# Kernel tuning notes

Measured on AMD Instinct MI355X. Metric: run time of the kernel, lower is better.

Reference implementation:

```python
import jax, jax.numpy as jnp
import numpy as np

EPS = 1e-5


def _layernorm(x, w, b):
    mu = jnp.mean(x, axis=-1, keepdims=True)
    var = jnp.var(x, axis=-1, keepdims=True)
    return (x - mu) * jax.lax.rsqrt(var + EPS) * w + b


def setup_inputs() -> dict:
    key = jax.random.key(0)
    ks = jax.random.split(key, 3)
    h, dff = 1024, 4096
    x = jax.random.normal(ks[0], (4, 2048, h), dtype=jnp.float32)
    w1 = jax.random.normal(ks[1], (h, dff), dtype=jnp.float32) * (1.0 / np.sqrt(h))
    w2 = jax.random.normal(ks[2], (dff, h), dtype=jnp.float32) * (1.0 / np.sqrt(dff))
    return {
        "x": x,
        "ln1_w": jnp.ones((h,), jnp.float32),
        "ln1_b": jnp.zeros((h,), jnp.float32),
        "ln2_w": jnp.ones((h,), jnp.float32),
        "ln2_b": jnp.zeros((h,), jnp.float32),
        "w1": w1,
        "b1": jnp.zeros((dff,), jnp.float32),
        "w2": w2,
        "b2": jnp.zeros((h,), jnp.float32),
    }


def reference(x, ln1_w, ln1_b, ln2_w, ln2_b, w1, b1, w2, b2):
    # double 1D FFT: over hidden (dim=-1) then sequence (dim=-2), keep real part
    fourier_x = jnp.fft.fft(jnp.fft.fft(x, axis=-1), axis=-2).real
    x = x + fourier_x
    x = _layernorm(x, ln1_w, ln1_b)
    # FFN: Linear -> exact GELU -> Linear (dropout is identity in eval)
    h = jax.nn.gelu(jnp.einsum("bsd,df->bsf", x, w1) + b1, approximate=False)
    x = x + jnp.einsum("bsf,fd->bsd", h, w2) + b2
    return _layernorm(x, ln2_w, ln2_b)
```

## Files before the change

kernel.cpp:

```cpp
#include <hip/hip_runtime.h>
#include <hip/hip_bf16.h>
#include <math.h>

typedef __bf16 bf16_t;
typedef __bf16 bf16x8 __attribute__((ext_vector_type(8)));
typedef __bf16 bf16x4 __attribute__((ext_vector_type(4)));
typedef float  f32x4  __attribute__((ext_vector_type(4)));

#define NROWS 8192
#define HD    1024
#define DFF   4096
#define HKEEP 513

typedef __attribute__((address_space(1))) const void* gas_cptr;
typedef __attribute__((address_space(3))) void* las_ptr;

__device__ __forceinline__ void gload_lds16(const void* g, void* l) {
  __builtin_amdgcn_global_load_lds((gas_cptr)g, (las_ptr)l, 16, 0, 0);
}

template <int N> __device__ __forceinline__ void vmw() {
  if      constexpr (N==4)  asm volatile("s_waitcnt vmcnt(4)"  ::: "memory");
  else if constexpr (N==6)  asm volatile("s_waitcnt vmcnt(6)"  ::: "memory");
}

__global__ __launch_bounds__(256) void transpose_to_bf16(
    const float* __restrict__ in, bf16_t* __restrict__ out, int R, int C)
{
  __shared__ float tile[32][33];
  const int bx = blockIdx.x, by = blockIdx.y;
  const int tx = threadIdx.x, ty = threadIdx.y;
  #pragma unroll
  for (int i = ty; i < 32; i += 8)
    tile[i][tx] = in[(size_t)(by*32 + i)*C + bx*32 + tx];
  __syncthreads();
  #pragma unroll
  for (int i = ty; i < 32; i += 8)
    out[(size_t)(bx*32 + i)*R + by*32 + tx] = (bf16_t)tile[tx][i];
}

#define RPB 16
#define LDW 1036
__global__ __launch_bounds__(512) void fft_h_t(
    const float* __restrict__ x, float* __restrict__ reT, float* __restrict__ imT)
{
  __shared__ float sre[8*LDW], sim[8*LDW], twc[512], tws[512];
  const int t = threadIdx.x;
  const int row0 = blockIdx.x * RPB;
  {
    float sv, cv; sincosf(-6.28318530717958647692f * (float)t * (1.0f/1024.0f), &sv, &cv);
    twc[t] = cv; tws[t] = sv;
  }
  #pragma unroll
  for (int q = 0; q < 4; ++q) {
    const int i = t + 512*q;
    const int pr = i >> 8;
    const int c4 = i & 255;
    float4 vr = *(const float4*)(x + (size_t)(row0 + 2*pr    )*HD + c4*4);
    float4 vi = *(const float4*)(x + (size_t)(row0 + 2*pr + 1)*HD + c4*4);
    *(float4*)&sre[pr*LDW + c4*4] = vr;
    *(float4*)&sim[pr*LDW + c4*4] = vi;
  }
  __syncthreads();
  const int b0i = __brev((unsigned)t) >> 22;
  const int b1i = __brev((unsigned)(t + 512)) >> 22;
  float rv[32];
  #pragma unroll
  for (int q = 0; q < 8; ++q) {
    rv[4*q]   = sre[q*LDW + b0i];
    rv[4*q+1] = sre[q*LDW + b1i];
    rv[4*q+2] = sim[q*LDW + b0i];
    rv[4*q+3] = sim[q*LDW + b1i];
  }
  __syncthreads();
  #pragma unroll
  for (int q = 0; q < 8; ++q) {
    sre[q*LDW + t]       = rv[4*q];
    sre[q*LDW + t + 512] = rv[4*q+1];
    sim[q*LDW + t]       = rv[4*q+2];
    sim[q*LDW + t + 512] = rv[4*q+3];
  }
  __syncthreads();
  for (int s = 0; s < 10; ++s) {
    const int half = 1 << s;
    const int j    = t & (half - 1);
    const int ib   = ((t >> s) << (s + 1)) | j;
    const int ti2  = j << (9 - s);
    const float wc = twc[ti2], ws = tws[ti2];
    #pragma unroll
    for (int q = 0; q < 8; ++q) {
      float* pr = &sre[q*LDW]; float* pi = &sim[q*LDW];
      const float r1 = pr[ib],      i1v = pi[ib];
      const float r2 = pr[ib+half], i2v = pi[ib+half];
      const float tr = r2*wc - i2v*ws;
      const float ti = r2*ws + i2v*wc;
      pr[ib]      = r1 + tr; pi[ib]      = i1v + ti;
      pr[ib+half] = r1 - tr; pi[ib+half] = i1v - ti;
    }
    __syncthreads();
  }
  const int tx = t & 15, th = t >> 4;
  const int q  = tx >> 1, par = tx & 1;
  #pragma unroll
  for (int hh = 0; hh < 17; ++hh) {
    const int h = hh*32 + th;
    if (h < HKEEP) {
      const int mh = (1024 - h) & 1023;
      const float zr = sre[q*LDW + h],  zi = sim[q*LDW + h];
      const float mr = sre[q*LDW + mh], mi = sim[q*LDW + mh];
      float orr, oii;
      if (par == 0) { orr = 0.5f*(zr + mr); oii = 0.5f*(zi - mi); }
      else          { orr = 0.5f*(zi + mi); oii = 0.5f*(mr - zr); }
      reT[(size_t)h*NROWS + row0 + tx] = orr;
      imT[(size_t)h*NROWS + row0 + tx] = oii;
    }
  }
}

__global__ __launch_bounds__(256) void fft_s_col(
    const float* __restrict__ reT, const float* __restrict__ imT,
    float* __restrict__ fT)
{
  __shared__ float sre[2048], sim[2048], twc[1024], tws[1024];
  const int t = threadIdx.x;
  const int h = blockIdx.x;
  const int batch = blockIdx.y;
  const size_t base = (size_t)h * NROWS + batch * 2048;
  for (int k = t; k < 1024; k += 256) {
    float sv, cv; sincosf(-6.28318530717958647692f * (float)k * (1.0f/2048.0f), &sv, &cv);
    twc[k] = cv; tws[k] = sv;
  }
  #pragma unroll
  for (int q = 0; q < 8; ++q) {
    const int i = t + 256*q;
    const int src = __brev((unsigned)i) >> 21;
    sre[i] = reT[base + src];
    sim[i] = imT[base + src];
  }
  __syncthreads();
  for (int s = 0; s < 11; ++s) {
    const int half = 1 << s;
    #pragma unroll
    for (int q = 0; q < 4; ++q) {
      const int b  = t + 256*q;
      const int j  = b & (half - 1);
      const int ib = ((b >> s) << (s + 1)) | j;
      const int ti2 = j << (10 - s);
      const float wc = twc[ti2], ws = tws[ti2];
      const float r1 = sre[ib],       i1v = sim[ib];
      const float r2 = sre[ib+half],  i2v = sim[ib+half];
      const float tr = r2*wc - i2v*ws;
      const float ti = r2*ws + i2v*wc;
      sre[ib]      = r1 + tr; sim[ib]      = i1v + ti;
      sre[ib+half] = r1 - tr; sim[ib+half] = i1v - ti;
    }
    __syncthreads();
  }
  #pragma unroll
  for (int q = 0; q < 8; ++q) {
    const int i = t + 256*q;
    fT[base + i] = sre[i];
  }
}

__global__ __launch_bounds__(256) void umadd_kernel(
    const float* __restrict__ fT, const float* __restrict__ x,
    float* __restrict__ y)
{
  __shared__ float tile[32][33];
  const int h0 = blockIdx.x * 32;
  const int b0 = blockIdx.y * 32;
  const int tx = threadIdx.x, ty = threadIdx.y;
  const int batch = b0 >> 11;
  const int s0    = b0 & 2047;
  #pragma unroll
  for (int i = ty; i < 32; i += 8) {
    const int h = h0 + i;
    float v;
    if (h <= 512) {
      v = fT[(size_t)h * NROWS + b0 + tx];
    } else {
      const int sp = (2048 - (s0 + tx)) & 2047;
      v = fT[(size_t)(1024 - h) * NROWS + (batch << 11) + sp];
    }
    tile[i][tx] = v;
  }
  __syncthreads();
  #pragma unroll
  for (int i = ty; i < 32; i += 8) {
    const size_t gi = (size_t)(b0+i)*HD + h0+tx;
    y[gi] = x[gi] + tile[tx][i];
  }
}

__global__ __launch_bounds__(256) void layernorm_f2b(
    const float* __restrict__ in, const float* __restrict__ gw,
    const float* __restrict__ gb, bf16_t* __restrict__ ob)
{
  __shared__ float red[8];
  const size_t row = blockIdx.x;
  const int t = threadIdx.x;
  const float* xr = in + row * HD;
  float4 v = *(const float4*)(xr + t*4);
  float s = v.x + v.y + v.z + v.w;
  #pragma unroll
  for (int o = 32; o > 0; o >>= 1) s += __shfl_xor(s, o);
  if ((t & 63) == 0) red[t >> 6] = s;
  __syncthreads();
  const float mu = (red[0]+red[1]+red[2]+red[3]) * (1.0f/1024.0f);
  const float dx = v.x-mu, dy = v.y-mu, dz = v.z-mu, dw = v.w-mu;
  float sq = dx*dx + dy*dy + dz*dz + dw*dw;
  #pragma unroll
  for (int o = 32; o > 0; o >>= 1) sq += __shfl_xor(sq, o);
  if ((t & 63) == 0) red[4 + (t >> 6)] = sq;
  __syncthreads();
  const float var  = (red[4]+red[5]+red[6]+red[7]) * (1.0f/1024.0f);
  const float rstd = rsqrtf(var + 1e-5f);
  const float4 wv = *(const float4*)(gw + t*4);
  const float4 bv = *(const float4*)(gb + t*4);
  bf16x4 o;
  o[0] = (bf16_t)(dx*rstd*wv.x + bv.x);
  o[1] = (bf16_t)(dy*rstd*wv.y + bv.y);
  o[2] = (bf16_t)(dz*rstd*wv.z + bv.z);
  o[3] = (bf16_t)(dw*rstd*wv.w + bv.w);
  *(bf16x4*)(ob + row*HD + t*4) = o;
}

__global__ __launch_bounds__(256) void layernorm_b2f(
    const bf16_t* __restrict__ in, const float* __restrict__ gw,
    const float* __restrict__ gb, float* __restrict__ of)
{
  __shared__ float red[8];
  const size_t row = blockIdx.x;
  const int t = threadIdx.x;
  bf16x4 v4 = *(const bf16x4*)(in + row*HD + t*4);
  const float vx = (float)v4[0], vy = (float)v4[1], vz = (float)v4[2], vw = (float)v4[3];
  float s = vx + vy + vz + vw;
  #pragma unroll
  for (int o = 32; o > 0; o >>= 1) s += __shfl_xor(s, o);
  if ((t & 63) == 0) red[t >> 6] = s;
  __syncthreads();
  const float mu = (red[0]+red[1]+red[2]+red[3]) * (1.0f/1024.0f);
  const float dx = vx-mu, dy = vy-mu, dz = vz-mu, dw = vw-mu;
  float sq = dx*dx + dy*dy + dz*dz + dw*dw;
  #pragma unroll
  for (int o = 32; o > 0; o >>= 1) sq += __shfl_xor(sq, o);
  if ((t & 63) == 0) red[4 + (t >> 6)] = sq;
  __syncthreads();
  const float var  = (red[4]+red[5]+red[6]+red[7]) * (1.0f/1024.0f);
  const float rstd = rsqrtf(var + 1e-5f);
  const float4 wv = *(const float4*)(gw + t*4);
  const float4 bv = *(const float4*)(gb + t*4);
  float4 o;
  o.x = dx*rstd*wv.x + bv.x;
  o.y = dy*rstd*wv.y + bv.y;
  o.z = dz*rstd*wv.z + bv.z;
  o.w = dw*rstd*wv.w + bv.w;
  *(float4*)(of + row*HD + t*4) = o;
}

__device__ __forceinline__ float gelu_fast(float v) {
  const float u  = 0.7978845608028654f * v * (1.0f + 0.044715f * v * v);
  const float e  = exp2f(-2.8853900817779268f * u);
  return v / (1.0f + e);
}

template <int NQ, bool GELU_OUT>
__global__ __launch_bounds__(512, 2) void gemm8r(
    const bf16_t* __restrict__ A,
    const bf16_t* __restrict__ Bt,
    const float*  __restrict__ bias,
    const bf16_t* __restrict__ resid,
    bf16_t* __restrict__ outB,
    int M, int N, int K, int gx)
{
  __shared__ bf16_t As[2][2][128*64];
  __shared__ bf16_t Bs[2][2][NQ*64*64];

  const int tid  = threadIdx.x;
  const int wave = tid >> 6, lane = tid & 63;
  const int wr = wave >> 2, wc = wave & 3;
  const int lr = lane & 15, lkg = lane >> 4;

  const int nwg = gridDim.x;
  const int sid = (blockIdx.x & 7) * (nwg >> 3) + (blockIdx.x >> 3);
  const int bx = sid % gx, by = sid / gx;
  const int brow = by * 256, bcol = bx * (NQ*128);

  const int rl = lane >> 3;
  const int sg = (lane & 7) ^ rl;

  auto stageA = [&](int b, int mh, int tt) {
    #pragma unroll
    for (int l = 0; l < 2; ++l) {
      const int row = brow + l*128 + mh*64 + wave*8 + rl;
      gload_lds16(A + (size_t)row * K + tt*64 + sg*8,
                  &As[b][mh][(l*64 + wave*8)*64]);
    }
  };
  auto stageB = [&](int b, int nh, int tt) {
    #pragma unroll
    for (int l = 0; l < NQ; ++l) {
      const int rho = l*64 + wave*8 + rl;
      const int wcs = rho / (NQ*16), r = rho % (NQ*16);
      const int row = bcol + wcs*(NQ*32) + nh*(NQ*16) + r;
      gload_lds16(Bt + (size_t)row * K + tt*64 + sg*8,
                  &Bs[b][nh][(l*64 + wave*8)*64]);
    }
  };

  f32x4 acc[8][2*NQ] = {};
  bf16x8 af[4][2];
  bf16x8 bq[2][NQ][2];

  const int NT = K >> 6;
  const int NI = NT >> 1;
  constexpr int WT = (NQ==2) ? 6 : 4;

  #define PHASE(BUF, MH, NH, DOA, DOB, STG, DOW) do { \
    if constexpr (DOA) { \
      _Pragma("unroll") for (int m = 0; m < 4; ++m) { \
      _Pragma("unroll") for (int ks = 0; ks < 2; ++ks) \
        af[m][ks] = *(const bf16x8*)&As[BUF][MH][(wr*64 + m*16 + lr)*64 + (((lkg + ks*4) ^ (lr & 7)) << 3)]; } \
    } \
    if constexpr (DOB) { \
      _Pragma("unroll") for (int n = 0; n < NQ; ++n) { \
      _Pragma("unroll") for (int ks = 0; ks < 2; ++ks) \
        bq[NH][n][ks] = *(const bf16x8*)&Bs[BUF][NH][(wc*(NQ*16) + n*16 + lr)*64 + (((lkg + ks*4) ^ (lr & 7)) << 3)]; } \
    } \
    STG; \
    __builtin_amdgcn_s_barrier(); \
    asm volatile("s_waitcnt lgkmcnt(0)" ::: "memory"); \
    __builtin_amdgcn_sched_barrier(0); \
    __builtin_amdgcn_s_setprio(1); \
    _Pragma("unroll") for (int m = 0; m < 4; ++m) { \
    _Pragma("unroll") for (int n = 0; n < NQ; ++n) { \
    _Pragma("unroll") for (int ks = 0; ks < 2; ++ks) \
      acc[(MH)*4+m][(NH)*NQ+n] = __builtin_amdgcn_mfma_f32_16x16x32_bf16(bq[NH][n][ks], af[m][ks], acc[(MH)*4+m][(NH)*NQ+n], 0, 0, 0); } } \
    __builtin_amdgcn_s_setprio(0); \
    if constexpr (DOW) vmw<WT>(); \
    __builtin_amdgcn_s_barrier(); \
  } while (0)

  stageB(0,0,0); stageA(0,0,0); stageB(0,1,0); stageA(0,1,0);
  stageB(1,0,1); stageA(1,0,1); stageB(1,1,1);
  vmw<WT>();
  __builtin_amdgcn_s_barrier();

  for (int j = 0; j < NI; ++j) {
    const int c1 = 2*j + 1;
    const int n2 = (2*j + 2 < NT) ? 2*j + 2 : NT - 1;
    const int n3 = (2*j + 3 < NT) ? 2*j + 3 : NT - 1;
    PHASE(0, 0, 0, 1, 1, stageA(1,1,c1), false);
    PHASE(0, 0, 1, 0, 1, stageB(0,0,n2), false);
    PHASE(0, 1, 1, 1, 0, stageA(0,0,n2), false);
    PHASE(0, 1, 0, 0, 0, stageB(0,1,n2), true);
    PHASE(1, 0, 0, 1, 1, stageA(0,1,n2), false);
    PHASE(1, 0, 1, 0, 1, stageB(1,0,n3), false);
    PHASE(1, 1, 1, 1, 0, stageA(1,0,n3), false);
    PHASE(1, 1, 0, 0, 0, stageB(1,1,n3), true);
  }
  #undef PHASE

  #pragma unroll
  for (int im = 0; im < 8; ++im) {
    const int row = brow + wr*128 + (im >> 2)*64 + (im & 3)*16 + lr;
    #pragma unroll
    for (int in = 0; in < 2*NQ; ++in) {
      const int col = bcol + wc*(NQ*32) + (in/NQ)*(NQ*16) + (in%NQ)*16 + lkg*4;
      const float4 bv4 = *(const float4*)(bias + col);
      float v0 = acc[im][in][0] + bv4.x;
      float v1 = acc[im][in][1] + bv4.y;
      float v2 = acc[im][in][2] + bv4.z;
      float v3 = acc[im][in][3] + bv4.w;
      bf16x4 o;
      if constexpr (GELU_OUT) {
        o[0] = (bf16_t)gelu_fast(v0); o[1] = (bf16_t)gelu_fast(v1);
        o[2] = (bf16_t)gelu_fast(v2); o[3] = (bf16_t)gelu_fast(v3);
      } else {
        bf16x4 rr = *(const bf16x4*)(resid + (size_t)row * N + col);
        o[0] = (bf16_t)(v0 + (float)rr[0]); o[1] = (bf16_t)(v1 + (float)rr[1]);
        o[2] = (bf16_t)(v2 + (float)rr[2]); o[3] = (bf16_t)(v3 + (float)rr[3]);
      }
      *(bf16x4*)(outB + (size_t)row * N + col) = o;
    }
  }
}

extern "C" void kernel_launch(void* const* d_in, const int* in_sizes, int n_in,
                              void* d_out, int out_size, void* d_ws, size_t ws_size,
                              hipStream_t stream) {
  const float* x    = (const float*)d_in[0];
  const float* ln1w = (const float*)d_in[1];
  const float* ln1b = (const float*)d_in[2];
  const float* ln2w = (const float*)d_in[3];
  const float* ln2b = (const float*)d_in[4];
  const float* w1   = (const float*)d_in[5];
  const float* b1   = (const float*)d_in[6];
  const float* w2   = (const float*)d_in[7];
  const float* b2   = (const float*)d_in[8];
  float* out = (float*)d_out;

  char* ws = (char*)d_ws;
  bf16_t* w1b = (bf16_t*)(ws);
  bf16_t* w2b = (bf16_t*)(ws + (8u   << 20));
  float*  reT = (float*) (ws + (16u  << 20));
  float*  imT = (float*) (ws + (33u  << 20));
  float*  fT  = (float*) (ws + (50u  << 20));
  float*  y   = (float*) (ws + (67u  << 20));
  bf16_t* xn  = (bf16_t*)(ws + (99u  << 20));
  bf16_t* hg  = (bf16_t*)(ws + (16u  << 20));
  bf16_t* z   = (bf16_t*)(ws + (80u  << 20));

  transpose_to_bf16<<<dim3(DFF/32, HD/32), dim3(32, 8), 0, stream>>>(w1, w1b, HD, DFF);
  transpose_to_bf16<<<dim3(HD/32, DFF/32), dim3(32, 8), 0, stream>>>(w2, w2b, DFF, HD);

  fft_h_t<<<NROWS/RPB, 512, 0, stream>>>(x, reT, imT);

  fft_s_col<<<dim3(513, 4), 256, 0, stream>>>(reT, imT, fT);

  umadd_kernel<<<dim3(HD/32, NROWS/32), dim3(32, 8), 0, stream>>>(fT, x, y);

  layernorm_f2b<<<NROWS, 256, 0, stream>>>(y, ln1w, ln1b, xn);

  gemm8r<2, true><<<(NROWS/256)*(DFF/256), 512, 0, stream>>>(
      xn, w1b, b1, nullptr, hg, NROWS, DFF, HD, DFF/256);
  gemm8r<1, false><<<(NROWS/256)*(HD/128), 512, 0, stream>>>(
      hg, w2b, b2, xn, z, NROWS, HD, DFF, HD/128);

  layernorm_b2f<<<NROWS, 256, 0, stream>>>(z, ln2w, ln2b, out);
}
```

Measured before the change: 286.9 us.

## Fuse FFT unmirror-add with LayerNorm1 and store FFT output in bf16

After: 276.8 us. -3.5%, faster.

```diff
diff --git a/kernel.cpp b/kernel.cpp
--- a/kernel.cpp
+++ b/kernel.cpp
@@ -119,7 +119,7 @@
 
 __global__ __launch_bounds__(256) void fft_s_col(
     const float* __restrict__ reT, const float* __restrict__ imT,
-    float* __restrict__ fT)
+    bf16_t* __restrict__ fTb)
 {
   __shared__ float sre[2048], sim[2048], twc[1024], tws[1024];
   const int t = threadIdx.x;
@@ -159,71 +159,72 @@
   #pragma unroll
   for (int q = 0; q < 8; ++q) {
     const int i = t + 256*q;
-    fT[base + i] = sre[i];
-  }
-}
-
-__global__ __launch_bounds__(256) void umadd_kernel(
-    const float* __restrict__ fT, const float* __restrict__ x,
-    float* __restrict__ y)
-{
-  __shared__ float tile[32][33];
-  const int h0 = blockIdx.x * 32;
-  const int b0 = blockIdx.y * 32;
-  const int tx = threadIdx.x, ty = threadIdx.y;
-  const int batch = b0 >> 11;
-  const int s0    = b0 & 2047;
-  #pragma unroll
-  for (int i = ty; i < 32; i += 8) {
-    const int h = h0 + i;
+    fTb[base + i] = (bf16_t)sre[i];
+  }
+}
+
+#define FLD 1028
+__global__ __launch_bounds__(256) void fuse_umadd_ln1(
+    const bf16_t* __restrict__ fTb, const float* __restrict__ x,
+    const float* __restrict__ gw, const float* __restrict__ gb,
+    bf16_t* __restrict__ xn)
+{
+  __shared__ float tile[16*FLD];
+  __shared__ float mrow[16], vrow[16];
+  const int t = threadIdx.x;
+  const int r0 = blockIdx.x * 16;
+  const int batch = r0 >> 11;
+  const int rb = t & 15;
+  const int hh = t >> 4;
+  const int rloc = (r0 + rb) & 2047;
+  const int sp = (2048 - rloc) & 2047;
+  #pragma unroll
+  for (int p = 0; p < 64; ++p) {
+    const int h = p*16 + hh;
     float v;
-    if (h <= 512) {
-      v = fT[(size_t)h * NROWS + b0 + tx];
-    } else {
-      const int sp = (2048 - (s0 + tx)) & 2047;
-      v = fT[(size_t)(1024 - h) * NROWS + (batch << 11) + sp];
-    }
-    tile[i][tx] = v;
-  }
-  __syncthreads();
-  #pragma unroll
-  for (int i = ty; i < 32; i += 8) {
-    const size_t gi = (size_t)(b0+i)*HD + h0+tx;
-    y[gi] = x[gi] + tile[tx][i];
-  }
-}
-
-__global__ __launch_bounds__(256) void layernorm_f2b(
-    const float* __restrict__ in, const float* __restrict__ gw,
-    const float* __restrict__ gb, bf16_t* __restrict__ ob)
-{
-  __shared__ float red[8];
-  const size_t row = blockIdx.x;
-  const int t = threadIdx.x;
-  const float* xr = in + row * HD;
-  float4 v = *(const float4*)(xr + t*4);
-  float s = v.x + v.y + v.z + v.w;
-  #pragma unroll
-  for (int o = 32; o > 0; o >>= 1) s += __shfl_xor(s, o);
-  if ((t & 63) == 0) red[t >> 6] = s;
-  __syncthreads();
-  const float mu = (red[0]+red[1]+red[2]+red[3]) * (1.0f/1024.0f);
-  const float dx = v.x-mu, dy = v.y-mu, dz = v.z-mu, dw = v.w-mu;
-  float sq = dx*dx + dy*dy + dz*dz + dw*dw;
-  #pragma unroll
-  for (int o = 32; o > 0; o >>= 1) sq += __shfl_xor(sq, o);
-  if ((t & 63) == 0) red[4 + (t >> 6)] = sq;
-  __syncthreads();
-  const float var  = (red[4]+red[5]+red[6]+red[7]) * (1.0f/1024.0f);
-  const float rstd = rsqrtf(var + 1e-5f);
+    if (h <= 512) v = (float)fTb[(size_t)h*NROWS + r0 + rb];
+    else          v = (float)fTb[(size_t)(1024-h)*NROWS + (batch<<11) + sp];
+    tile[rb*FLD + h] = v;
+  }
+  __syncthreads();
+  #pragma unroll
+  for (int rr = 0; rr < 16; ++rr) {
+    float4 xv = *(const float4*)(x + (size_t)(r0+rr)*HD + t*4);
+    float4 tv = *(float4*)&tile[rr*FLD + t*4];
+    tv.x += xv.x; tv.y += xv.y; tv.z += xv.z; tv.w += xv.w;
+    *(float4*)&tile[rr*FLD + t*4] = tv;
+  }
+  __syncthreads();
+  {
+    const int r = t >> 4, i = t & 15;
+    float s = 0.f, s2 = 0.f;
+    #pragma unroll
+    for (int k = 0; k < 64; ++k) {
+      const float v = tile[r*FLD + i + 16*k];
+      s += v; s2 += v*v;
+    }
+    #pragma unroll
+    for (int o = 8; o > 0; o >>= 1) { s += __shfl_xor(s, o); s2 += __shfl_xor(s2, o); }
+    if (i == 0) {
+      const float mu = s * (1.0f/1024.0f);
+      mrow[r] = mu;
+      vrow[r] = rsqrtf(s2 * (1.0f/1024.0f) - mu*mu + 1e-5f);
+    }
+  }
+  __syncthreads();
   const float4 wv = *(const float4*)(gw + t*4);
   const float4 bv = *(const float4*)(gb + t*4);
-  bf16x4 o;
-  o[0] = (bf16_t)(dx*rstd*wv.x + bv.x);
-  o[1] = (bf16_t)(dy*rstd*wv.y + bv.y);
-  o[2] = (bf16_t)(dz*rstd*wv.z + bv.z);
-  o[3] = (bf16_t)(dw*rstd*wv.w + bv.w);
-  *(bf16x4*)(ob + row*HD + t*4) = o;
+  #pragma unroll
+  for (int rr = 0; rr < 16; ++rr) {
+    const float mu = mrow[rr], rs = vrow[rr];
+    float4 tv = *(float4*)&tile[rr*FLD + t*4];
+    bf16x4 o;
+    o[0] = (bf16_t)((tv.x-mu)*rs*wv.x + bv.x);
+    o[1] = (bf16_t)((tv.y-mu)*rs*wv.y + bv.y);
+    o[2] = (bf16_t)((tv.z-mu)*rs*wv.z + bv.z);
+    o[3] = (bf16_t)((tv.w-mu)*rs*wv.w + bv.w);
+    *(bf16x4*)(xn + (size_t)(r0+rr)*HD + t*4) = o;
+  }
 }
 
 __global__ __launch_bounds__(256) void layernorm_b2f(
@@ -406,8 +407,7 @@
   bf16_t* w2b = (bf16_t*)(ws + (8u   << 20));
   float*  reT = (float*) (ws + (16u  << 20));
   float*  imT = (float*) (ws + (33u  << 20));
-  float*  fT  = (float*) (ws + (50u  << 20));
-  float*  y   = (float*) (ws + (67u  << 20));
+  bf16_t* fTb = (bf16_t*)(ws + (50u  << 20));
   bf16_t* xn  = (bf16_t*)(ws + (99u  << 20));
   bf16_t* hg  = (bf16_t*)(ws + (16u  << 20));
   bf16_t* z   = (bf16_t*)(ws + (80u  << 20));
@@ -417,11 +417,9 @@
 
   fft_h_t<<<NROWS/RPB, 512, 0, stream>>>(x, reT, imT);
 
-  fft_s_col<<<dim3(513, 4), 256, 0, stream>>>(reT, imT, fT);
-
-  umadd_kernel<<<dim3(HD/32, NROWS/32), dim3(32, 8), 0, stream>>>(fT, x, y);
-
-  layernorm_f2b<<<NROWS, 256, 0, stream>>>(y, ln1w, ln1b, xn);
+  fft_s_col<<<dim3(513, 4), 256, 0, stream>>>(reT, imT, fTb);
+
+  fuse_umadd_ln1<<<NROWS/16, 256, 0, stream>>>(fTb, x, ln1w, ln1b, xn);
 
   gemm8r<2, true><<<(NROWS/256)*(DFF/256), 512, 0, stream>>>(
       xn, w1b, b1, nullptr, hg, NROWS, DFF, HD, DFF/256);
```
